# Kernel tuning notes

Hardware: AMD Instinct MI355X
Metric: run time of the kernel (lower is better)

## Reference

```python
import jax, jax.numpy as jnp
import numpy as np

N_HIDDEN = 1024
N_INPUTS = 8
N_OUTPUTS = 8
BATCH = 32
SEQ_LEN = 1000
DT = 0.001
TAU = 0.01
TAU_DEPR = 0.2
TAU_FACIL = 1.5
BETA = 10.0
PROB_C = 0.1


def setup_inputs() -> dict:
    key = jax.random.key(0)
    ks = jax.random.split(key, 9)
    # gain adjustment from source: 1/(0.5/(1+beta*0.5*tau_depr)) = 4.0 -> gain = 6.4
    gain = 1.6 * (1.0 / (0.5 / (1.0 + BETA * 0.5 * TAU_DEPR)))
    x = jax.random.normal(ks[0], (BATCH, SEQ_LEN, N_INPUTS), dtype=jnp.float32)
    h_0 = jax.random.normal(ks[1], (BATCH, N_HIDDEN), dtype=jnp.float32)
    r_0 = jax.random.uniform(ks[2], (BATCH, N_HIDDEN), dtype=jnp.float32)
    u_0 = jax.random.uniform(ks[3], (BATCH, N_HIDDEN), dtype=jnp.float32)
    p_rel = jax.random.uniform(ks[4], (N_HIDDEN,), minval=0.1, maxval=0.9, dtype=jnp.float32)
    presyn_scaling = jnp.ones((N_HIDDEN,), dtype=jnp.float32)
    W_ih = jax.random.normal(ks[5], (N_HIDDEN, N_INPUTS), dtype=jnp.float32) / np.sqrt(N_HIDDEN)
    W_hh = jax.random.normal(ks[6], (N_HIDDEN, N_HIDDEN), dtype=jnp.float32) * (gain / np.sqrt(PROB_C * N_HIDDEN))
    W_hh_mask = jax.random.bernoulli(ks[7], PROB_C, (N_HIDDEN, N_HIDDEN)).astype(jnp.float32)
    W_hz = jax.random.normal(ks[8], (N_OUTPUTS, N_HIDDEN), dtype=jnp.float32) / np.sqrt(N_HIDDEN)
    return {"x": x, "h_0": h_0, "r_0": r_0, "u_0": u_0, "p_rel": p_rel,
            "presyn_scaling": presyn_scaling, "W_ih": W_ih, "W_hh": W_hh,
            "W_hh_mask": W_hh_mask, "W_hz": W_hz}


def reference(x, h_0, r_0, u_0, p_rel, presyn_scaling, W_ih, W_hh, W_hh_mask, W_hz):
    # noise_std = 0.0 in source -> noise term is identically zero.
    W_eff = W_hh * W_hh_mask                       # [n, n], eff[i,j] applied to presyn j
    x_proj = jnp.einsum('bti,ni->btn', x, W_ih)    # precompute input drive [b, t, n]

    def step(carry, x_t):
        h_prev, r_prev, u_prev, h_tr = carry       # each [b, n]
        drive = 0.5 * (1.0 + h_tr)                 # presynaptic activity
        r_t = r_prev + ((p_rel - r_prev) / TAU_DEPR - BETA * r_prev * drive) * DT
        u_t = u_prev + ((p_rel - u_prev) / TAU_FACIL + BETA * (1.0 - u_prev) * drive) * DT
        # h_tr @ (r_prev * scal * W_hh * mask).T == (r_prev * scal * h_tr) @ W_eff.T
        rec = (r_prev * presyn_scaling * h_tr) @ W_eff.T
        h_t = h_prev + ((-h_prev + x_t + rec) / TAU) * DT
        h_tr_new = jnp.tanh(h_t)
        z_t = h_tr_new @ W_hz.T                    # [b, n_outputs]
        return (h_t, r_t, u_t, h_tr_new), (z_t, h_t, r_t, u_t)

    init = (h_0, r_0, u_0, jnp.tanh(h_0))
    _, (z, h, r, u) = jax.lax.scan(step, init, jnp.swapaxes(x_proj, 0, 1))
    # scan stacks on time axis 0 -> transpose back to [b, t, ...]
    to_bt = lambda a: jnp.swapaxes(a, 0, 1)
    return (to_bt(z), to_bt(h), to_bt(r), to_bt(u))
```

## Files before the change

kernel.cpp:

```cpp
#include <hip/hip_runtime.h>
#include <math.h>

#define NH 1024
#define NB 32
#define NI 8
#define NO 8
#define TSTEPS 1000

#define NWG 256
#define BLK 512
#define NG 8
#define NM 32
#define GBATCH 4

#define OFF_Z 0
#define OFF_H (NB * TSTEPS * NO)
#define OFF_R (OFF_H + NB * TSTEPS * NH)
#define OFF_U (OFF_R + NB * TSTEPS * NH)

#define WS_A  8192
#define WS_ZP (WS_A + 2 * NG * NH * GBATCH)

typedef unsigned long long u64;

__device__ __forceinline__ float2 aload2(const float* p) {
    u64 v = __hip_atomic_load((const u64*)p, __ATOMIC_RELAXED,
                              __HIP_MEMORY_SCOPE_AGENT);
    return __builtin_bit_cast(float2, v);
}
__device__ __forceinline__ float aload1(const float* p) {
    return __hip_atomic_load(p, __ATOMIC_RELAXED, __HIP_MEMORY_SCOPE_AGENT);
}
__device__ __forceinline__ void astore(float* p, float v) {
    __hip_atomic_store(p, v, __ATOMIC_RELAXED, __HIP_MEMORY_SCOPE_AGENT);
}

__device__ __forceinline__ void groupbar(unsigned* slot, int G, int m,
                                         unsigned stamp) {
    __syncthreads();
    if (threadIdx.x == 0)
        __hip_atomic_store(&slot[(G * NM + m) * 32], stamp,
                           __ATOMIC_RELAXED, __HIP_MEMORY_SCOPE_AGENT);
    if (threadIdx.x < NM) {
        while (__hip_atomic_load(&slot[(G * NM + threadIdx.x) * 32],
                                 __ATOMIC_RELAXED, __HIP_MEMORY_SCOPE_AGENT)
               < stamp)
            __builtin_amdgcn_s_sleep(1);
    }
    __syncthreads();
}

__global__ __launch_bounds__(BLK, 2) void rnn_stp_kernel(
    const float* __restrict__ x,
    const float* __restrict__ h0,
    const float* __restrict__ r0,
    const float* __restrict__ u0,
    const float* __restrict__ prel,
    const float* __restrict__ scal,
    const float* __restrict__ Wih,
    const float* __restrict__ Whh,
    const float* __restrict__ Wmask,
    const float* __restrict__ Whz,
    float* __restrict__ out,
    float* __restrict__ ws)
{
    const int tid = threadIdx.x;
    const int g   = blockIdx.x;

    const int G = g & 7;
    const int m = g >> 3;

    unsigned* slot = (unsigned*)ws;
    float* Abuf = ws + WS_A;
    float* ZP   = ws + WS_ZP;

    const int ib = 32 * m;

    __shared__ float4 atile[NM * 33];
    __shared__ float  red[8 * 16 * 9];
    __shared__ float  hbuf[GBATCH][NM];

    const int lane = tid & 63, wid = tid >> 6;

    const int ks = tid >> 4;
    const int il = tid & 15;

    float w[2][32];
    #pragma unroll
    for (int nn = 0; nn < 2; ++nn) {
        const int row = 32 * m + il + 16 * nn;
        const float* wp = Whh   + row * NH + 32 * ks;
        const float* mp = Wmask + row * NH + 32 * ks;
        #pragma unroll
        for (int jj = 0; jj < 32; ++jj) w[nn][jj] = wp[jj] * mp[jj];
    }

    const bool own = tid < 128;
    const int ob = tid >> 5;
    const int on = tid & 31;
    const int bglob = G * GBATCH + ob;
    const int oi = ib + on;
    float h = 0.f, r = 0.f, u = 0.f, htr = 0.f, p = 0.f, sc = 0.f;
    float wih[8];
    if (own) {
        h  = h0[bglob * NH + oi];
        r  = r0[bglob * NH + oi];
        u  = u0[bglob * NH + oi];
        p  = prel[oi];
        sc = scal[oi];
        #pragma unroll
        for (int k = 0; k < 8; ++k) wih[k] = Wih[oi * NI + k];
        htr = tanhf(h);
        astore(&Abuf[G * (NH * GBATCH) + oi * GBATCH + ob], r * sc * htr);
    }

    float wzv[4];
    #pragma unroll
    for (int k = 0; k < 4; ++k)
        wzv[k] = Whz[(lane >> 3) * NH + ib + (lane & 7) + 8 * k];
    const int bf = m >> 3, of = m & 7;

    unsigned stamp = 1;
    groupbar(slot, G, m, stamp); ++stamp;

    for (int t = 0; t < TSTEPS; ++t) {
        const int par = t & 1;

        const float* Ag = Abuf + par * (NG * NH * GBATCH) + G * (NH * GBATCH);
        {
            float2 s0 = aload2(Ag + tid * 8 + 0);
            float2 s1 = aload2(Ag + tid * 8 + 2);
            float2 s2 = aload2(Ag + tid * 8 + 4);
            float2 s3 = aload2(Ag + tid * 8 + 6);
            const int r0i = tid * 2;
            atile[r0i + (r0i >> 5)]     = make_float4(s0.x, s0.y, s1.x, s1.y);
            atile[r0i + 1 + (r0i >> 5)] = make_float4(s2.x, s2.y, s3.x, s3.y);
        }

        float4 xa = make_float4(0.f, 0.f, 0.f, 0.f), xb = xa;
        if (own) {
            const float4* xp = (const float4*)(x + (bglob * TSTEPS + t) * NI);
            xa = xp[0];
            xb = xp[1];
        }
        __syncthreads();

        float acc[2][4] = {{0.f,0.f,0.f,0.f},{0.f,0.f,0.f,0.f}};
        {
            const float4* at4 = atile + 33 * ks;
            #pragma unroll
            for (int jj = 0; jj < 32; ++jj) {
                float4 a = at4[jj];
                const float w0 = w[0][jj], w1 = w[1][jj];
                acc[0][0] = fmaf(a.x, w0, acc[0][0]);
                acc[0][1] = fmaf(a.y, w0, acc[0][1]);
                acc[0][2] = fmaf(a.z, w0, acc[0][2]);
                acc[0][3] = fmaf(a.w, w0, acc[0][3]);
                acc[1][0] = fmaf(a.x, w1, acc[1][0]);
                acc[1][1] = fmaf(a.y, w1, acc[1][1]);
                acc[1][2] = fmaf(a.z, w1, acc[1][2]);
                acc[1][3] = fmaf(a.w, w1, acc[1][3]);
            }
        }

        #pragma unroll
        for (int mm = 16; mm <= 32; mm <<= 1) {
            #pragma unroll
            for (int nn = 0; nn < 2; ++nn) {
                #pragma unroll
                for (int q = 0; q < 4; ++q)
                    acc[nn][q] += __shfl_xor(acc[nn][q], mm, 64);
            }
        }
        if (lane < 16) {
            float* rp = red + (wid * 16 + lane) * 9;
            rp[0] = acc[0][0]; rp[1] = acc[0][1];
            rp[2] = acc[0][2]; rp[3] = acc[0][3];
            rp[4] = acc[1][0]; rp[5] = acc[1][1];
            rp[6] = acc[1][2]; rp[7] = acc[1][3];
        }
        __syncthreads();

        if (own) {
            float rec = 0.f;
            #pragma unroll
            for (int wv = 0; wv < 8; ++wv)
                rec += red[(wv * 16 + (on & 15)) * 9 + (on >> 4) * 4 + ob];

            float xv = fmaf(xa.x, wih[0], fmaf(xa.y, wih[1],
                       fmaf(xa.z, wih[2], xa.w * wih[3])));
            xv = fmaf(xb.x, wih[4], fmaf(xb.y, wih[5],
                 fmaf(xb.z, wih[6], fmaf(xb.w, wih[7], xv))));

            float drive = 0.5f * (1.0f + htr);
            float rn = r + ((p - r) / 0.2f - 10.0f * r * drive) * 0.001f;
            float un = u + ((p - u) / 1.5f + 10.0f * (1.0f - u) * drive) * 0.001f;
            float hn = h + ((-h + xv + rec) / 0.01f) * 0.001f;
            float htn = tanhf(hn);

            out[OFF_H + (bglob * TSTEPS + t) * NH + oi] = hn;
            out[OFF_R + (bglob * TSTEPS + t) * NH + oi] = rn;
            out[OFF_U + (bglob * TSTEPS + t) * NH + oi] = un;

            astore(&Abuf[(par ^ 1) * (NG * NH * GBATCH) + G * (NH * GBATCH)
                         + oi * GBATCH + ob], rn * sc * htn);
            hbuf[ob][on] = htn;

            h = hn; r = rn; u = un; htr = htn;
        }
        __syncthreads();

        if (wid < 4) {
            const int o = lane >> 3, ns = lane & 7;
            float zp = 0.f;
            #pragma unroll
            for (int k = 0; k < 4; ++k)
                zp = fmaf(hbuf[wid][ns + 8 * k], wzv[k], zp);
            zp += __shfl_xor(zp, 1, 64);
            zp += __shfl_xor(zp, 2, 64);
            zp += __shfl_xor(zp, 4, 64);
            if (ns == 0)
                astore(&ZP[par * (NG * GBATCH * NO * NM)
                           + G * (GBATCH * NO * NM)
                           + wid * (NO * NM) + o * NM + m], zp);
        }
        if (t >= 1 && wid == 4 && lane < NM) {
            float v = aload1(ZP + (par ^ 1) * (NG * GBATCH * NO * NM)
                             + G * (GBATCH * NO * NM)
                             + bf * (NO * NM) + of * NM + lane);
            v += __shfl_xor(v, 1, 64);
            v += __shfl_xor(v, 2, 64);
            v += __shfl_xor(v, 4, 64);
            v += __shfl_xor(v, 8, 64);
            v += __shfl_xor(v, 16, 64);
            if (lane == 0)
                out[OFF_Z + ((G * GBATCH + bf) * TSTEPS + (t - 1)) * NO + of] = v;
        }

        groupbar(slot, G, m, stamp); ++stamp;
    }

    if (wid == 4 && lane < NM) {
        float v = aload1(ZP + 1 * (NG * GBATCH * NO * NM)
                         + G * (GBATCH * NO * NM)
                         + bf * (NO * NM) + of * NM + lane);
        v += __shfl_xor(v, 1, 64);
        v += __shfl_xor(v, 2, 64);
        v += __shfl_xor(v, 4, 64);
        v += __shfl_xor(v, 8, 64);
        v += __shfl_xor(v, 16, 64);
        if (lane == 0)
            out[OFF_Z + ((G * GBATCH + bf) * TSTEPS + 999) * NO + of] = v;
    }
}

extern "C" void kernel_launch(void* const* d_in, const int* in_sizes, int n_in,
                              void* d_out, int out_size, void* d_ws, size_t ws_size,
                              hipStream_t stream) {
    const float* x     = (const float*)d_in[0];
    const float* h0    = (const float*)d_in[1];
    const float* r0    = (const float*)d_in[2];
    const float* u0    = (const float*)d_in[3];
    const float* prel  = (const float*)d_in[4];
    const float* scal  = (const float*)d_in[5];
    const float* Wih   = (const float*)d_in[6];
    const float* Whh   = (const float*)d_in[7];
    const float* Wmask = (const float*)d_in[8];
    const float* Whz   = (const float*)d_in[9];
    float* out = (float*)d_out;
    float* ws  = (float*)d_ws;

    hipMemsetAsync(d_ws, 0, NWG * 128, stream);

    void* args[] = { &x, &h0, &r0, &u0, &prel, &scal,
                     &Wih, &Whh, &Wmask, &Whz, &out, &ws };
    hipLaunchCooperativeKernel((void*)rnn_stp_kernel, dim3(NWG), dim3(BLK),
                               args, 0, stream);
}
```

Measured before the change: 3.834 ms.

## Split group barrier into arrive/wait and fuse output projection into owner threads

Replaces the per-step group barrier (syncthreads, stamp, spin, syncthreads) with a split arrive-after-step and wait-at-top-of-next-step scheme, where each wave polls four peer slots in parallel. The W_hz output projection now runs in the owner threads via warp shuffles with W_hz staged in LDS, which removes the hbuf stage and one syncthreads. The final z read is moved into the matmul phase. This cuts barrier latency on the critical path of the serial recurrence, at the cost of relying on relaxed atomics with no explicit fences for ordering.

```diff
diff --git a/kernel.cpp b/kernel.cpp
--- a/kernel.cpp
+++ b/kernel.cpp
@@ -33,21 +33,6 @@
 }
 __device__ __forceinline__ void astore(float* p, float v) {
     __hip_atomic_store(p, v, __ATOMIC_RELAXED, __HIP_MEMORY_SCOPE_AGENT);
-}
-
-__device__ __forceinline__ void groupbar(unsigned* slot, int G, int m,
-                                         unsigned stamp) {
-    __syncthreads();
-    if (threadIdx.x == 0)
-        __hip_atomic_store(&slot[(G * NM + m) * 32], stamp,
-                           __ATOMIC_RELAXED, __HIP_MEMORY_SCOPE_AGENT);
-    if (threadIdx.x < NM) {
-        while (__hip_atomic_load(&slot[(G * NM + threadIdx.x) * 32],
-                                 __ATOMIC_RELAXED, __HIP_MEMORY_SCOPE_AGENT)
-               < stamp)
-            __builtin_amdgcn_s_sleep(1);
-    }
-    __syncthreads();
 }
 
 __global__ __launch_bounds__(BLK, 2) void rnn_stp_kernel(
@@ -78,9 +63,12 @@
 
     __shared__ float4 atile[NM * 33];
     __shared__ float  red[8 * 16 * 9];
-    __shared__ float  hbuf[GBATCH][NM];
+    __shared__ float  wzlds[NM * 8];
 
     const int lane = tid & 63, wid = tid >> 6;
+
+    if (tid < NM * 8)
+        wzlds[(tid >> 3) * 8 + (tid & 7)] = Whz[(tid & 7) * NH + ib + (tid >> 3)];
 
     const int ks = tid >> 4;
     const int il = tid & 15;
@@ -114,17 +102,23 @@
         astore(&Abuf[G * (NH * GBATCH) + oi * GBATCH + ob], r * sc * htr);
     }
 
-    float wzv[4];
-    #pragma unroll
-    for (int k = 0; k < 4; ++k)
-        wzv[k] = Whz[(lane >> 3) * NH + ib + (lane & 7) + 8 * k];
     const int bf = m >> 3, of = m & 7;
 
-    unsigned stamp = 1;
-    groupbar(slot, G, m, stamp); ++stamp;
+    __syncthreads();
+    if (tid == 0)
+        __hip_atomic_store(&slot[(G * NM + m) * 32], 1u,
+                           __ATOMIC_RELAXED, __HIP_MEMORY_SCOPE_AGENT);
+
+    const unsigned* myslot = &slot[(G * NM + 4 * wid + (lane & 3)) * 32];
 
     for (int t = 0; t < TSTEPS; ++t) {
         const int par = t & 1;
+
+        if (lane < 4) {
+            while (__hip_atomic_load(myslot, __ATOMIC_RELAXED,
+                                     __HIP_MEMORY_SCOPE_AGENT) < (unsigned)(t + 1))
+                __builtin_amdgcn_s_sleep(1);
+        }
 
         const float* Ag = Abuf + par * (NG * NH * GBATCH) + G * (NH * GBATCH);
         {
@@ -144,6 +138,12 @@
             xb = xp[1];
         }
         __syncthreads();
+
+        float zfin = 0.f;
+        if (t >= 1 && wid == 4 && lane < NM)
+            zfin = aload1(ZP + (par ^ 1) * (NG * GBATCH * NO * NM)
+                          + G * (GBATCH * NO * NM)
+                          + bf * (NO * NM) + of * NM + lane);
 
         float acc[2][4] = {{0.f,0.f,0.f,0.f},{0.f,0.f,0.f,0.f}};
         {
@@ -179,6 +179,16 @@
             rp[4] = acc[1][0]; rp[5] = acc[1][1];
             rp[6] = acc[1][2]; rp[7] = acc[1][3];
         }
+
+        if (t >= 1 && wid == 4) {
+            zfin += __shfl_xor(zfin, 1, 64);
+            zfin += __shfl_xor(zfin, 2, 64);
+            zfin += __shfl_xor(zfin, 4, 64);
+            zfin += __shfl_xor(zfin, 8, 64);
+            zfin += __shfl_xor(zfin, 16, 64);
+            if (lane == 0)
+                out[OFF_Z + ((G * GBATCH + bf) * TSTEPS + (t - 1)) * NO + of] = zfin;
+        }
         __syncthreads();
 
         if (own) {
@@ -204,46 +214,44 @@
 
             astore(&Abuf[(par ^ 1) * (NG * NH * GBATCH) + G * (NH * GBATCH)
                          + oi * GBATCH + ob], rn * sc * htn);
-            hbuf[ob][on] = htn;
+
+            float zp[8];
+            #pragma unroll
+            for (int o = 0; o < 8; ++o) zp[o] = htn * wzlds[on * 8 + o];
+            #pragma unroll
+            for (int mm = 1; mm <= 16; mm <<= 1) {
+                #pragma unroll
+                for (int o = 0; o < 8; ++o)
+                    zp[o] += __shfl_xor(zp[o], mm, 64);
+            }
+            if (on == 0) {
+                float* zpp = ZP + par * (NG * GBATCH * NO * NM)
+                             + G * (GBATCH * NO * NM) + ob * (NO * NM) + m;
+                #pragma unroll
+                for (int o = 0; o < 8; ++o) astore(zpp + o * NM, zp[o]);
+            }
 
             h = hn; r = rn; u = un; htr = htn;
         }
+
         __syncthreads();
-
-        if (wid < 4) {
-            const int o = lane >> 3, ns = lane & 7;
-            float zp = 0.f;
-            #pragma unroll
-            for (int k = 0; k < 4; ++k)
-                zp = fmaf(hbuf[wid][ns + 8 * k], wzv[k], zp);
-            zp += __shfl_xor(zp, 1, 64);
-            zp += __shfl_xor(zp, 2, 64);
-            zp += __shfl_xor(zp, 4, 64);
-            if (ns == 0)
-                astore(&ZP[par * (NG * GBATCH * NO * NM)
-                           + G * (GBATCH * NO * NM)
-                           + wid * (NO * NM) + o * NM + m], zp);
-        }
-        if (t >= 1 && wid == 4 && lane < NM) {
-            float v = aload1(ZP + (par ^ 1) * (NG * GBATCH * NO * NM)
-                             + G * (GBATCH * NO * NM)
-                             + bf * (NO * NM) + of * NM + lane);
-            v += __shfl_xor(v, 1, 64);
-            v += __shfl_xor(v, 2, 64);
-            v += __shfl_xor(v, 4, 64);
-            v += __shfl_xor(v, 8, 64);
-            v += __shfl_xor(v, 16, 64);
-            if (lane == 0)
-                out[OFF_Z + ((G * GBATCH + bf) * TSTEPS + (t - 1)) * NO + of] = v;
-        }
-
-        groupbar(slot, G, m, stamp); ++stamp;
-    }
-
-    if (wid == 4 && lane < NM) {
-        float v = aload1(ZP + 1 * (NG * GBATCH * NO * NM)
-                         + G * (GBATCH * NO * NM)
-                         + bf * (NO * NM) + of * NM + lane);
+        if (tid == 0)
+            __hip_atomic_store(&slot[(G * NM + m) * 32], (unsigned)(t + 2),
+                               __ATOMIC_RELAXED, __HIP_MEMORY_SCOPE_AGENT);
+    }
+
+    if (lane < 4) {
+        while (__hip_atomic_load(myslot, __ATOMIC_RELAXED,
+                                 __HIP_MEMORY_SCOPE_AGENT) < (unsigned)(TSTEPS + 1))
+            __builtin_amdgcn_s_sleep(1);
+    }
+    __syncthreads();
+    if (wid == 4) {
+        float v = 0.f;
+        if (lane < NM)
+            v = aload1(ZP + 1 * (NG * GBATCH * NO * NM)
+                       + G * (GBATCH * NO * NM)
+                       + bf * (NO * NM) + of * NM + lane);
         v += __shfl_xor(v, 1, 64);
         v += __shfl_xor(v, 2, 64);
         v += __shfl_xor(v, 4, 64);
```

New measurement: 4.216 ms. 1.1x slower.

## Add 512-workgroup variant with two batches per group and occupancy-based dispatch

Applied to the files above, without the earlier changes.

Adds a kernel variant that splits the batch into 16 groups of 2 instead of 8 groups of 4, using 512 workgroups (two per CU). Each workgroup then computes a smaller per-step matmul and has fewer owner threads, which shortens the serial critical path of each timestep. The host checks occupancy and launches the new variant with a normal launch instead of a cooperative one, falling back to the old kernel otherwise. Without a cooperative launch, co-residency of all workgroups is not guaranteed, so the spin barriers could deadlock. The Z reduction is also moved ahead of the partial-product write to change the step schedule.

```diff
diff --git a/kernel.cpp b/kernel.cpp
--- a/kernel.cpp
+++ b/kernel.cpp
@@ -7,20 +7,11 @@
 #define NO 8
 #define TSTEPS 1000
 
-#define NWG 256
-#define BLK 512
-#define NG 8
-#define NM 32
-#define GBATCH 4
-
 #define OFF_Z 0
 #define OFF_H (NB * TSTEPS * NO)
 #define OFF_R (OFF_H + NB * TSTEPS * NH)
 #define OFF_U (OFF_R + NB * TSTEPS * NH)
 
-#define WS_A  8192
-#define WS_ZP (WS_A + 2 * NG * NH * GBATCH)
-
 typedef unsigned long long u64;
 
 __device__ __forceinline__ float2 aload2(const float* p) {
@@ -35,14 +26,21 @@
     __hip_atomic_store(p, v, __ATOMIC_RELAXED, __HIP_MEMORY_SCOPE_AGENT);
 }
 
-__device__ __forceinline__ void groupbar(unsigned* slot, int G, int m,
-                                         unsigned stamp) {
+#define A_NWG 512
+#define A_NG 16
+#define A_NM 32
+#define A_GB 2
+#define A_WS_A  16384
+#define A_WS_ZP (A_WS_A + 2 * A_NG * NH * A_GB)
+
+__device__ __forceinline__ void groupbar_a(unsigned* slot, int G, int m,
+                                           unsigned stamp) {
     __syncthreads();
     if (threadIdx.x == 0)
-        __hip_atomic_store(&slot[(G * NM + m) * 32], stamp,
+        __hip_atomic_store(&slot[(G * A_NM + m) * 32], stamp,
                            __ATOMIC_RELAXED, __HIP_MEMORY_SCOPE_AGENT);
-    if (threadIdx.x < NM) {
-        while (__hip_atomic_load(&slot[(G * NM + threadIdx.x) * 32],
+    if (threadIdx.x < A_NM) {
+        while (__hip_atomic_load(&slot[(G * A_NM + threadIdx.x) * 32],
                                  __ATOMIC_RELAXED, __HIP_MEMORY_SCOPE_AGENT)
                < stamp)
             __builtin_amdgcn_s_sleep(1);
@@ -50,35 +48,29 @@
     __syncthreads();
 }
 
-__global__ __launch_bounds__(BLK, 2) void rnn_stp_kernel(
-    const float* __restrict__ x,
-    const float* __restrict__ h0,
-    const float* __restrict__ r0,
-    const float* __restrict__ u0,
-    const float* __restrict__ prel,
-    const float* __restrict__ scal,
-    const float* __restrict__ Wih,
-    const float* __restrict__ Whh,
-    const float* __restrict__ Wmask,
-    const float* __restrict__ Whz,
-    float* __restrict__ out,
-    float* __restrict__ ws)
+__global__ __launch_bounds__(512, 2) void rnn_stp_kernel_a(
+    const float* __restrict__ x,  const float* __restrict__ h0,
+    const float* __restrict__ r0, const float* __restrict__ u0,
+    const float* __restrict__ prel, const float* __restrict__ scal,
+    const float* __restrict__ Wih,  const float* __restrict__ Whh,
+    const float* __restrict__ Wmask, const float* __restrict__ Whz,
+    float* __restrict__ out, float* __restrict__ ws)
 {
     const int tid = threadIdx.x;
     const int g   = blockIdx.x;
 
-    const int G = g & 7;
-    const int m = g >> 3;
+    const int G = g >> 5;
+    const int m = g & 31;
 
     unsigned* slot = (unsigned*)ws;
-    float* Abuf = ws + WS_A;
-    float* ZP   = ws + WS_ZP;
+    float* Abuf = ws + A_WS_A;
+    float* ZP   = ws + A_WS_ZP;
 
     const int ib = 32 * m;
 
-    __shared__ float4 atile[NM * 33];
-    __shared__ float  red[8 * 16 * 9];
-    __shared__ float  hbuf[GBATCH][NM];
+    __shared__ float2 atile[NH + A_NM];
+    __shared__ float  red[8 * 16 * 5];
+    __shared__ float  hbuf[A_GB][A_NM];
 
     const int lane = tid & 63, wid = tid >> 6;
 
@@ -95,10 +87,10 @@
         for (int jj = 0; jj < 32; ++jj) w[nn][jj] = wp[jj] * mp[jj];
     }
 
-    const bool own = tid < 128;
+    const bool own = tid < 64;
     const int ob = tid >> 5;
     const int on = tid & 31;
-    const int bglob = G * GBATCH + ob;
+    const int bglob = G * A_GB + ob;
     const int oi = ib + on;
     float h = 0.f, r = 0.f, u = 0.f, htr = 0.f, p = 0.f, sc = 0.f;
     float wih[8];
@@ -111,7 +103,221 @@
         #pragma unroll
         for (int k = 0; k < 8; ++k) wih[k] = Wih[oi * NI + k];
         htr = tanhf(h);
-        astore(&Abuf[G * (NH * GBATCH) + oi * GBATCH + ob], r * sc * htr);
+        astore(&Abuf[G * (NH * A_GB) + oi * A_GB + ob], r * sc * htr);
+    }
+
+    float wzv[4];
+    #pragma unroll
+    for (int k = 0; k < 4; ++k)
+        wzv[k] = Whz[(lane >> 3) * NH + ib + (lane & 7) + 8 * k];
+    const int bf = (m >> 3) & 1, of = m & 7;
+
+    unsigned stamp = 1;
+    groupbar_a(slot, G, m, stamp); ++stamp;
+
+    for (int t = 0; t < TSTEPS; ++t) {
+        const int par = t & 1;
+
+        const float* Ag = Abuf + par * (A_NG * NH * A_GB) + G * (NH * A_GB);
+        {
+            float2 s0 = aload2(Ag + (2 * tid) * 2);
+            float2 s1 = aload2(Ag + (2 * tid + 1) * 2);
+            const int r0i = 2 * tid;
+            atile[r0i + (r0i >> 5)]     = s0;
+            atile[r0i + 1 + (r0i >> 5)] = s1;
+        }
+
+        float4 xa = make_float4(0.f, 0.f, 0.f, 0.f), xb = xa;
+        if (own) {
+            const float4* xp = (const float4*)(x + (bglob * TSTEPS + t) * NI);
+            xa = xp[0];
+            xb = xp[1];
+        }
+        __syncthreads();
+
+        float acc[2][2] = {{0.f, 0.f}, {0.f, 0.f}};
+        {
+            const float2* at2 = atile + 33 * ks;
+            #pragma unroll
+            for (int jj = 0; jj < 32; ++jj) {
+                float2 a = at2[jj];
+                const float w0 = w[0][jj], w1 = w[1][jj];
+                acc[0][0] = fmaf(a.x, w0, acc[0][0]);
+                acc[0][1] = fmaf(a.y, w0, acc[0][1]);
+                acc[1][0] = fmaf(a.x, w1, acc[1][0]);
+                acc[1][1] = fmaf(a.y, w1, acc[1][1]);
+            }
+        }
+
+        #pragma unroll
+        for (int mm = 16; mm <= 32; mm <<= 1) {
+            #pragma unroll
+            for (int nn = 0; nn < 2; ++nn) {
+                #pragma unroll
+                for (int q = 0; q < 2; ++q)
+                    acc[nn][q] += __shfl_xor(acc[nn][q], mm, 64);
+            }
+        }
+        if (lane < 16) {
+            float* rp = red + (wid * 16 + lane) * 5;
+            rp[0] = acc[0][0]; rp[1] = acc[0][1];
+            rp[2] = acc[1][0]; rp[3] = acc[1][1];
+        }
+        __syncthreads();
+
+        if (own) {
+            float rec = 0.f;
+            #pragma unroll
+            for (int wv = 0; wv < 8; ++wv)
+                rec += red[(wv * 16 + (on & 15)) * 5 + (on >> 4) * 2 + ob];
+
+            float xv = fmaf(xa.x, wih[0], fmaf(xa.y, wih[1],
+                       fmaf(xa.z, wih[2], xa.w * wih[3])));
+            xv = fmaf(xb.x, wih[4], fmaf(xb.y, wih[5],
+                 fmaf(xb.z, wih[6], fmaf(xb.w, wih[7], xv))));
+
+            float drive = 0.5f * (1.0f + htr);
+            float rn = r + ((p - r) / 0.2f - 10.0f * r * drive) * 0.001f;
+            float un = u + ((p - u) / 1.5f + 10.0f * (1.0f - u) * drive) * 0.001f;
+            float hn = h + ((-h + xv + rec) / 0.01f) * 0.001f;
+            float htn = tanhf(hn);
+
+            out[OFF_H + (bglob * TSTEPS + t) * NH + oi] = hn;
+            out[OFF_R + (bglob * TSTEPS + t) * NH + oi] = rn;
+            out[OFF_U + (bglob * TSTEPS + t) * NH + oi] = un;
+
+            astore(&Abuf[(par ^ 1) * (A_NG * NH * A_GB) + G * (NH * A_GB)
+                         + oi * A_GB + ob], rn * sc * htn);
+            hbuf[ob][on] = htn;
+
+            h = hn; r = rn; u = un; htr = htn;
+        }
+        if (t >= 1 && wid == 4 && m < 16 && lane < A_NM) {
+            float v = aload1(ZP + (par ^ 1) * (A_NG * A_GB * NO * A_NM)
+                             + G * (A_GB * NO * A_NM)
+                             + bf * (NO * A_NM) + of * A_NM + lane);
+            v += __shfl_xor(v, 1, 64);
+            v += __shfl_xor(v, 2, 64);
+            v += __shfl_xor(v, 4, 64);
+            v += __shfl_xor(v, 8, 64);
+            v += __shfl_xor(v, 16, 64);
+            if (lane == 0)
+                out[OFF_Z + ((G * A_GB + bf) * TSTEPS + (t - 1)) * NO + of] = v;
+        }
+        __syncthreads();
+
+        if (wid < A_GB) {
+            const int o = lane >> 3, ns = lane & 7;
+            float zp = 0.f;
+            #pragma unroll
+            for (int k = 0; k < 4; ++k)
+                zp = fmaf(hbuf[wid][ns + 8 * k], wzv[k], zp);
+            zp += __shfl_xor(zp, 1, 64);
+            zp += __shfl_xor(zp, 2, 64);
+            zp += __shfl_xor(zp, 4, 64);
+            if (ns == 0)
+                astore(&ZP[par * (A_NG * A_GB * NO * A_NM)
+                           + G * (A_GB * NO * A_NM)
+                           + wid * (NO * A_NM) + o * A_NM + m], zp);
+        }
+
+        groupbar_a(slot, G, m, stamp); ++stamp;
+    }
+
+    if (wid == 4 && m < 16) {
+        float v = 0.f;
+        if (lane < A_NM)
+            v = aload1(ZP + 1 * (A_NG * A_GB * NO * A_NM)
+                       + G * (A_GB * NO * A_NM)
+                       + bf * (NO * A_NM) + of * A_NM + lane);
+        v += __shfl_xor(v, 1, 64);
+        v += __shfl_xor(v, 2, 64);
+        v += __shfl_xor(v, 4, 64);
+        v += __shfl_xor(v, 8, 64);
+        v += __shfl_xor(v, 16, 64);
+        if (lane == 0)
+            out[OFF_Z + ((G * A_GB + bf) * TSTEPS + 999) * NO + of] = v;
+    }
+}
+
+#define B_NWG 256
+#define B_NG 8
+#define B_NM 32
+#define B_GB 4
+#define B_WS_A  8192
+#define B_WS_ZP (B_WS_A + 2 * B_NG * NH * B_GB)
+
+__device__ __forceinline__ void groupbar_b(unsigned* slot, int G, int m,
+                                           unsigned stamp) {
+    __syncthreads();
+    if (threadIdx.x == 0)
+        __hip_atomic_store(&slot[(G * B_NM + m) * 32], stamp,
+                           __ATOMIC_RELAXED, __HIP_MEMORY_SCOPE_AGENT);
+    if (threadIdx.x < B_NM) {
+        while (__hip_atomic_load(&slot[(G * B_NM + threadIdx.x) * 32],
+                                 __ATOMIC_RELAXED, __HIP_MEMORY_SCOPE_AGENT)
+               < stamp)
+            __builtin_amdgcn_s_sleep(1);
+    }
+    __syncthreads();
+}
+
+__global__ __launch_bounds__(512, 2) void rnn_stp_kernel_b(
+    const float* __restrict__ x,  const float* __restrict__ h0,
+    const float* __restrict__ r0, const float* __restrict__ u0,
+    const float* __restrict__ prel, const float* __restrict__ scal,
+    const float* __restrict__ Wih,  const float* __restrict__ Whh,
+    const float* __restrict__ Wmask, const float* __restrict__ Whz,
+    float* __restrict__ out, float* __restrict__ ws)
+{
+    const int tid = threadIdx.x;
+    const int g   = blockIdx.x;
+
+    const int G = g & 7;
+    const int m = g >> 3;
+
+    unsigned* slot = (unsigned*)ws;
+    float* Abuf = ws + B_WS_A;
+    float* ZP   = ws + B_WS_ZP;
+
+    const int ib = 32 * m;
+
+    __shared__ float4 atile[B_NM * 33];
+    __shared__ float  red[8 * 16 * 9];
+    __shared__ float  hbuf[B_GB][B_NM];
+
+    const int lane = tid & 63, wid = tid >> 6;
+
+    const int ks = tid >> 4;
+    const int il = tid & 15;
+
+    float w[2][32];
+    #pragma unroll
+    for (int nn = 0; nn < 2; ++nn) {
+        const int row = 32 * m + il + 16 * nn;
+        const float* wp = Whh   + row * NH + 32 * ks;
+        const float* mp = Wmask + row * NH + 32 * ks;
+        #pragma unroll
+        for (int jj = 0; jj < 32; ++jj) w[nn][jj] = wp[jj] * mp[jj];
+    }
+
+    const bool own = tid < 128;
+    const int ob = tid >> 5;
+    const int on = tid & 31;
+    const int bglob = G * B_GB + ob;
+    const int oi = ib + on;
+    float h = 0.f, r = 0.f, u = 0.f, htr = 0.f, p = 0.f, sc = 0.f;
+    float wih[8];
+    if (own) {
+        h  = h0[bglob * NH + oi];
+        r  = r0[bglob * NH + oi];
+        u  = u0[bglob * NH + oi];
+        p  = prel[oi];
+        sc = scal[oi];
+        #pragma unroll
+        for (int k = 0; k < 8; ++k) wih[k] = Wih[oi * NI + k];
+        htr = tanhf(h);
+        astore(&Abuf[G * (NH * B_GB) + oi * B_GB + ob], r * sc * htr);
     }
 
     float wzv[4];
@@ -121,12 +327,12 @@
     const int bf = m >> 3, of = m & 7;
 
     unsigned stamp = 1;
-    groupbar(slot, G, m, stamp); ++stamp;
+    groupbar_b(slot, G, m, stamp); ++stamp;
 
     for (int t = 0; t < TSTEPS; ++t) {
         const int par = t & 1;
 
-        const float* Ag = Abuf + par * (NG * NH * GBATCH) + G * (NH * GBATCH);
+        const float* Ag = Abuf + par * (B_NG * NH * B_GB) + G * (NH * B_GB);
         {
             float2 s0 = aload2(Ag + tid * 8 + 0);
             float2 s1 = aload2(Ag + tid * 8 + 2);
@@ -202,8 +408,8 @@
             out[OFF_R + (bglob * TSTEPS + t) * NH + oi] = rn;
             out[OFF_U + (bglob * TSTEPS + t) * NH + oi] = un;
 
-            astore(&Abuf[(par ^ 1) * (NG * NH * GBATCH) + G * (NH * GBATCH)
-                         + oi * GBATCH + ob], rn * sc * htn);
+            astore(&Abuf[(par ^ 1) * (B_NG * NH * B_GB) + G * (NH * B_GB)
+                         + oi * B_GB + ob], rn * sc * htn);
             hbuf[ob][on] = htn;
 
             h = hn; r = rn; u = un; htr = htn;
@@ -220,37 +426,37 @@
             zp += __shfl_xor(zp, 2, 64);
             zp += __shfl_xor(zp, 4, 64);
             if (ns == 0)
-                astore(&ZP[par * (NG * GBATCH * NO * NM)
-                           + G * (GBATCH * NO * NM)
-                           + wid * (NO * NM) + o * NM + m], zp);
-        }
-        if (t >= 1 && wid == 4 && lane < NM) {
-            float v = aload1(ZP + (par ^ 1) * (NG * GBATCH * NO * NM)
-                             + G * (GBATCH * NO * NM)
-                             + bf * (NO * NM) + of * NM + lane);
+                astore(&ZP[par * (B_NG * B_GB * NO * B_NM)
+                           + G * (B_GB * NO * B_NM)
+                           + wid * (NO * B_NM) + o * B_NM + m], zp);
+        }
+        if (t >= 1 && wid == 4 && lane < B_NM) {
+            float v = aload1(ZP + (par ^ 1) * (B_NG * B_GB * NO * B_NM)
+                             + G * (B_GB * NO * B_NM)
+                             + bf * (NO * B_NM) + of * B_NM + lane);
             v += __shfl_xor(v, 1, 64);
             v += __shfl_xor(v, 2, 64);
             v += __shfl_xor(v, 4, 64);
             v += __shfl_xor(v, 8, 64);
             v += __shfl_xor(v, 16, 64);
             if (lane == 0)
-                out[OFF_Z + ((G * GBATCH + bf) * TSTEPS + (t - 1)) * NO + of] = v;
-        }
-
-        groupbar(slot, G, m, stamp); ++stamp;
-    }
-
-    if (wid == 4 && lane < NM) {
-        float v = aload1(ZP + 1 * (NG * GBATCH * NO * NM)
-                         + G * (GBATCH * NO * NM)
-                         + bf * (NO * NM) + of * NM + lane);
+                out[OFF_Z + ((G * B_GB + bf) * TSTEPS + (t - 1)) * NO + of] = v;
+        }
+
+        groupbar_b(slot, G, m, stamp); ++stamp;
+    }
+
+    if (wid == 4 && lane < B_NM) {
+        float v = aload1(ZP + 1 * (B_NG * B_GB * NO * B_NM)
+                         + G * (B_GB * NO * B_NM)
+                         + bf * (NO * B_NM) + of * B_NM + lane);
         v += __shfl_xor(v, 1, 64);
         v += __shfl_xor(v, 2, 64);
         v += __shfl_xor(v, 4, 64);
         v += __shfl_xor(v, 8, 64);
         v += __shfl_xor(v, 16, 64);
         if (lane == 0)
-            out[OFF_Z + ((G * GBATCH + bf) * TSTEPS + 999) * NO + of] = v;
+            out[OFF_Z + ((G * B_GB + bf) * TSTEPS + 999) * NO + of] = v;
     }
 }
 
@@ -270,10 +476,20 @@
     float* out = (float*)d_out;
     float* ws  = (float*)d_ws;
 
-    hipMemsetAsync(d_ws, 0, NWG * 128, stream);
-
-    void* args[] = { &x, &h0, &r0, &u0, &prel, &scal,
-                     &Wih, &Whh, &Wmask, &Whz, &out, &ws };
-    hipLaunchCooperativeKernel((void*)rnn_stp_kernel, dim3(NWG), dim3(BLK),
-                               args, 0, stream);
-}
+    int occ = 0;
+    hipError_t e = hipOccupancyMaxActiveBlocksPerMultiprocessor(
+        &occ, (const void*)rnn_stp_kernel_a, 512, 0);
+    const bool useA = (e == hipSuccess) && (occ >= 2);
+
+    if (useA) {
+        hipMemsetAsync(d_ws, 0, A_NWG * 128, stream);
+        rnn_stp_kernel_a<<<dim3(A_NWG), dim3(512), 0, stream>>>(
+            x, h0, r0, u0, prel, scal, Wih, Whh, Wmask, Whz, out, ws);
+    } else {
+        hipMemsetAsync(d_ws, 0, B_NWG * 128, stream);
+        void* args[] = { &x, &h0, &r0, &u0, &prel, &scal,
+                         &Wih, &Whh, &Wmask, &Whz, &out, &ws };
+        hipLaunchCooperativeKernel((void*)rnn_stp_kernel_b, dim3(B_NWG),
+                                   dim3(512), args, 0, stream);
+    }
+}
```

After: 3.815 ms. No clear change (-0.5%).

## Split batch into 16 groups of 2 across 512 workgroups

Applied to the files above, without the earlier changes.

Doubles the workgroup count so each group handles 2 batch rows instead of 4. This halves per-workgroup matvec work and the global A-tile load per step, and every WG still keeps its slice of W_hh in registers. The z readout is moved ahead of the block sync, the kernel switches from a cooperative launch to a plain one, and the z-reduction reads are restricted to m<16. The risks are that 512 WGs with launch bounds of 2 per CU must all be co-resident for the spin barrier to work, and that more workgroups now take part in each group barrier.

```diff
diff --git a/kernel.cpp b/kernel.cpp
--- a/kernel.cpp
+++ b/kernel.cpp
@@ -7,19 +7,19 @@
 #define NO 8
 #define TSTEPS 1000
 
-#define NWG 256
+#define NWG 512
 #define BLK 512
-#define NG 8
+#define NG 16
 #define NM 32
-#define GBATCH 4
+#define GB 2
 
 #define OFF_Z 0
 #define OFF_H (NB * TSTEPS * NO)
 #define OFF_R (OFF_H + NB * TSTEPS * NH)
 #define OFF_U (OFF_R + NB * TSTEPS * NH)
 
-#define WS_A  8192
-#define WS_ZP (WS_A + 2 * NG * NH * GBATCH)
+#define WS_A  16384
+#define WS_ZP (WS_A + 2 * NG * NH * GB)
 
 typedef unsigned long long u64;
 
@@ -67,8 +67,8 @@
     const int tid = threadIdx.x;
     const int g   = blockIdx.x;
 
-    const int G = g & 7;
-    const int m = g >> 3;
+    const int G = g >> 5;
+    const int m = g & 31;
 
     unsigned* slot = (unsigned*)ws;
     float* Abuf = ws + WS_A;
@@ -76,9 +76,9 @@
 
     const int ib = 32 * m;
 
-    __shared__ float4 atile[NM * 33];
-    __shared__ float  red[8 * 16 * 9];
-    __shared__ float  hbuf[GBATCH][NM];
+    __shared__ float2 atile[NH + NM];
+    __shared__ float  red[8 * 16 * 5];
+    __shared__ float  hbuf[GB][NM];
 
     const int lane = tid & 63, wid = tid >> 6;
 
@@ -95,10 +95,10 @@
         for (int jj = 0; jj < 32; ++jj) w[nn][jj] = wp[jj] * mp[jj];
     }
 
-    const bool own = tid < 128;
+    const bool own = tid < 64;
     const int ob = tid >> 5;
     const int on = tid & 31;
-    const int bglob = G * GBATCH + ob;
+    const int bglob = G * GB + ob;
     const int oi = ib + on;
     float h = 0.f, r = 0.f, u = 0.f, htr = 0.f, p = 0.f, sc = 0.f;
     float wih[8];
@@ -111,14 +111,14 @@
         #pragma unroll
         for (int k = 0; k < 8; ++k) wih[k] = Wih[oi * NI + k];
         htr = tanhf(h);
-        astore(&Abuf[G * (NH * GBATCH) + oi * GBATCH + ob], r * sc * htr);
+        astore(&Abuf[G * (NH * GB) + oi * GB + ob], r * sc * htr);
     }
 
     float wzv[4];
     #pragma unroll
     for (int k = 0; k < 4; ++k)
         wzv[k] = Whz[(lane >> 3) * NH + ib + (lane & 7) + 8 * k];
-    const int bf = m >> 3, of = m & 7;
+    const int bf = (m >> 3) & 1, of = m & 7;
 
     unsigned stamp = 1;
     groupbar(slot, G, m, stamp); ++stamp;
@@ -126,15 +126,13 @@
     for (int t = 0; t < TSTEPS; ++t) {
         const int par = t & 1;
 
-        const float* Ag = Abuf + par * (NG * NH * GBATCH) + G * (NH * GBATCH);
+        const float* Ag = Abuf + par * (NG * NH * GB) + G * (NH * GB);
         {
-            float2 s0 = aload2(Ag + tid * 8 + 0);
-            float2 s1 = aload2(Ag + tid * 8 + 2);
-            float2 s2 = aload2(Ag + tid * 8 + 4);
-            float2 s3 = aload2(Ag + tid * 8 + 6);
-            const int r0i = tid * 2;
-            atile[r0i + (r0i >> 5)]     = make_float4(s0.x, s0.y, s1.x, s1.y);
-            atile[r0i + 1 + (r0i >> 5)] = make_float4(s2.x, s2.y, s3.x, s3.y);
+            float2 s0 = aload2(Ag + (2 * tid) * 2);
+            float2 s1 = aload2(Ag + (2 * tid + 1) * 2);
+            const int r0i = 2 * tid;
+            atile[r0i + (r0i >> 5)]     = s0;
+            atile[r0i + 1 + (r0i >> 5)] = s1;
         }
 
         float4 xa = make_float4(0.f, 0.f, 0.f, 0.f), xb = xa;
@@ -145,21 +143,17 @@
         }
         __syncthreads();
 
-        float acc[2][4] = {{0.f,0.f,0.f,0.f},{0.f,0.f,0.f,0.f}};
+        float acc[2][2] = {{0.f, 0.f}, {0.f, 0.f}};
         {
-            const float4* at4 = atile + 33 * ks;
+            const float2* at2 = atile + 33 * ks;
             #pragma unroll
             for (int jj = 0; jj < 32; ++jj) {
-                float4 a = at4[jj];
+                float2 a = at2[jj];
                 const float w0 = w[0][jj], w1 = w[1][jj];
                 acc[0][0] = fmaf(a.x, w0, acc[0][0]);
                 acc[0][1] = fmaf(a.y, w0, acc[0][1]);
-                acc[0][2] = fmaf(a.z, w0, acc[0][2]);
-                acc[0][3] = fmaf(a.w, w0, acc[0][3]);
                 acc[1][0] = fmaf(a.x, w1, acc[1][0]);
                 acc[1][1] = fmaf(a.y, w1, acc[1][1]);
-                acc[1][2] = fmaf(a.z, w1, acc[1][2]);
-                acc[1][3] = fmaf(a.w, w1, acc[1][3]);
             }
         }
 
@@ -168,16 +162,14 @@
             #pragma unroll
             for (int nn = 0; nn < 2; ++nn) {
                 #pragma unroll
-                for (int q = 0; q < 4; ++q)
+                for (int q = 0; q < 2; ++q)
                     acc[nn][q] += __shfl_xor(acc[nn][q], mm, 64);
             }
         }
         if (lane < 16) {
-            float* rp = red + (wid * 16 + lane) * 9;
+            float* rp = red + (wid * 16 + lane) * 5;
             rp[0] = acc[0][0]; rp[1] = acc[0][1];
-            rp[2] = acc[0][2]; rp[3] = acc[0][3];
-            rp[4] = acc[1][0]; rp[5] = acc[1][1];
-            rp[6] = acc[1][2]; rp[7] = acc[1][3];
+            rp[2] = acc[1][0]; rp[3] = acc[1][1];
         }
         __syncthreads();
 
@@ -185,7 +177,7 @@
             float rec = 0.f;
             #pragma unroll
             for (int wv = 0; wv < 8; ++wv)
-                rec += red[(wv * 16 + (on & 15)) * 9 + (on >> 4) * 4 + ob];
+                rec += red[(wv * 16 + (on & 15)) * 5 + (on >> 4) * 2 + ob];
 
             float xv = fmaf(xa.x, wih[0], fmaf(xa.y, wih[1],
                        fmaf(xa.z, wih[2], xa.w * wih[3])));
@@ -202,31 +194,15 @@
             out[OFF_R + (bglob * TSTEPS + t) * NH + oi] = rn;
             out[OFF_U + (bglob * TSTEPS + t) * NH + oi] = un;
 
-            astore(&Abuf[(par ^ 1) * (NG * NH * GBATCH) + G * (NH * GBATCH)
-                         + oi * GBATCH + ob], rn * sc * htn);
+            astore(&Abuf[(par ^ 1) * (NG * NH * GB) + G * (NH * GB)
+                         + oi * GB + ob], rn * sc * htn);
             hbuf[ob][on] = htn;
 
             h = hn; r = rn; u = un; htr = htn;
         }
-        __syncthreads();
-
-        if (wid < 4) {
-            const int o = lane >> 3, ns = lane & 7;
-            float zp = 0.f;
-            #pragma unroll
-            for (int k = 0; k < 4; ++k)
-                zp = fmaf(hbuf[wid][ns + 8 * k], wzv[k], zp);
-            zp += __shfl_xor(zp, 1, 64);
-            zp += __shfl_xor(zp, 2, 64);
-            zp += __shfl_xor(zp, 4, 64);
-            if (ns == 0)
-                astore(&ZP[par * (NG * GBATCH * NO * NM)
-                           + G * (GBATCH * NO * NM)
-                           + wid * (NO * NM) + o * NM + m], zp);
-        }
-        if (t >= 1 && wid == 4 && lane < NM) {
-            float v = aload1(ZP + (par ^ 1) * (NG * GBATCH * NO * NM)
-                             + G * (GBATCH * NO * NM)
+        if (t >= 1 && wid == 4 && m < 16 && lane < NM) {
+            float v = aload1(ZP + (par ^ 1) * (NG * GB * NO * NM)
+                             + G * (GB * NO * NM)
                              + bf * (NO * NM) + of * NM + lane);
             v += __shfl_xor(v, 1, 64);
             v += __shfl_xor(v, 2, 64);
@@ -234,23 +210,41 @@
             v += __shfl_xor(v, 8, 64);
             v += __shfl_xor(v, 16, 64);
             if (lane == 0)
-                out[OFF_Z + ((G * GBATCH + bf) * TSTEPS + (t - 1)) * NO + of] = v;
+                out[OFF_Z + ((G * GB + bf) * TSTEPS + (t - 1)) * NO + of] = v;
+        }
+        __syncthreads();
+
+        if (wid < GB) {
+            const int o = lane >> 3, ns = lane & 7;
+            float zp = 0.f;
+            #pragma unroll
+            for (int k = 0; k < 4; ++k)
+                zp = fmaf(hbuf[wid][ns + 8 * k], wzv[k], zp);
+            zp += __shfl_xor(zp, 1, 64);
+            zp += __shfl_xor(zp, 2, 64);
+            zp += __shfl_xor(zp, 4, 64);
+            if (ns == 0)
+                astore(&ZP[par * (NG * GB * NO * NM)
+                           + G * (GB * NO * NM)
+                           + wid * (NO * NM) + o * NM + m], zp);
         }
 
         groupbar(slot, G, m, stamp); ++stamp;
     }
 
-    if (wid == 4 && lane < NM) {
-        float v = aload1(ZP + 1 * (NG * GBATCH * NO * NM)
-                         + G * (GBATCH * NO * NM)
-                         + bf * (NO * NM) + of * NM + lane);
+    if (wid == 4 && m < 16) {
+        float v = 0.f;
+        if (lane < NM)
+            v = aload1(ZP + 1 * (NG * GB * NO * NM)
+                       + G * (GB * NO * NM)
+                       + bf * (NO * NM) + of * NM + lane);
         v += __shfl_xor(v, 1, 64);
         v += __shfl_xor(v, 2, 64);
         v += __shfl_xor(v, 4, 64);
         v += __shfl_xor(v, 8, 64);
         v += __shfl_xor(v, 16, 64);
         if (lane == 0)
-            out[OFF_Z + ((G * GBATCH + bf) * TSTEPS + 999) * NO + of] = v;
+            out[OFF_Z + ((G * GB + bf) * TSTEPS + 999) * NO + of] = v;
     }
 }
 
@@ -272,8 +266,6 @@
 
     hipMemsetAsync(d_ws, 0, NWG * 128, stream);
 
-    void* args[] = { &x, &h0, &r0, &u0, &prel, &scal,
-                     &Wih, &Whh, &Wmask, &Whz, &out, &ws };
-    hipLaunchCooperativeKernel((void*)rnn_stp_kernel, dim3(NWG), dim3(BLK),
-                               args, 0, stream);
-}
+    rnn_stp_kernel<<<dim3(NWG), dim3(BLK), 0, stream>>>(
+        x, h0, r0, u0, prel, scal, Wih, Whh, Wmask, Whz, out, ws);
+}
```

Result: slower. 6.978 ms (+82.0%).
